# Performance work log

Measured on AMD Instinct MI355X. Metric: run time of the kernel, lower is better.

Reference implementation:

```python
import jax, jax.numpy as jnp
import numpy as np
from jax import lax

T, B, H, Q = 4096, 64, 128, 1024
K = 31                 # convolution_filter_size
PAD = (K - 1) // 2     # alignment_conv_padding = 15
WL = 128               # window_length


def setup_inputs() -> dict:
    key = jax.random.key(0)
    ks = jax.random.split(key, 8)
    return {
        "encoded_tokens": jax.random.normal(ks[0], (T, B, H), jnp.float32),
        "tokens_mask": jnp.ones((B, T), dtype=bool),
        "num_tokens": jnp.full((B,), T, dtype=jnp.int32),
        "query": jax.random.normal(ks[1], (1, B, Q), jnp.float32),
        "cumulative_alignment": jax.random.uniform(ks[2], (B, T), jnp.float32),
        "initial_cumulative_alignment": jax.random.uniform(ks[3], (B, 1), jnp.float32),
        "window_start": jax.random.randint(ks[4], (B,), 0, T - WL, dtype=jnp.int32),
        "Wq": jax.random.normal(ks[5], (H, Q), jnp.float32) * 0.02,
        "bq": jnp.zeros((H,), jnp.float32),
        "conv_w": jax.random.normal(ks[6], (H, 1, K), jnp.float32) * 0.1,
        "conv_b": jnp.zeros((H,), jnp.float32),
        "v": jax.random.normal(ks[7], (H,), jnp.float32) * 0.1,
    }


def reference(encoded_tokens, tokens_mask, num_tokens, query,
              cumulative_alignment, initial_cumulative_alignment, window_start,
              Wq, bq, conv_w, conv_b, v):
    Tn, Bn, Hn = encoded_tokens.shape
    W = min(WL, Tn)

    # mask padded positions of cumulative alignment
    cum = jnp.where(tokens_mask, cumulative_alignment, 0.0)          # [B, T]

    # left-pad with initial_cumulative_alignment, right-pad with zeros
    left = jnp.broadcast_to(initial_cumulative_alignment[..., None], (Bn, 1, PAD))
    loc = jnp.concatenate([left, cum[:, None, :]], axis=-1)          # [B, 1, T+PAD]
    loc = jnp.pad(loc, ((0, 0), (0, 0), (0, PAD)))                   # [B, 1, T+2*PAD]

    # variable-offset windows (gather)
    win_idx = window_start[:, None] + jnp.arange(W)                  # [B, W]
    mask_w = jnp.take_along_axis(tokens_mask, win_idx, axis=1)       # [B, W]
    enc_w = jax.vmap(lambda e, s: lax.dynamic_slice_in_dim(e, s, W, axis=0),
                     in_axes=(1, 0), out_axes=1)(encoded_tokens, window_start)  # [W, B, H]
    loc_w = jax.vmap(lambda l, s: lax.dynamic_slice_in_dim(l, s, W + 2 * PAD, axis=0),
                     in_axes=(0, 0))(loc[:, 0, :], window_start)     # [B, W+2*PAD]

    # location conv (valid padding) -> [B, H, W]
    feats = lax.conv_general_dilated(loc_w[:, None, :], conv_w, (1,), 'VALID',
                                     dimension_numbers=('NCH', 'OIH', 'NCH'))
    feats = feats + conv_b[None, :, None]

    # query projection and additive scoring
    qp = query[0] @ Wq.T + bq                                        # [B, H]
    feats = jnp.tanh(feats + qp[:, :, None])                         # [B, H, W]
    score = jnp.einsum('bhw,h->bw', feats, v)                        # [B, W]
    score = jnp.where(mask_w, score, -jnp.inf)
    align_w = jax.nn.softmax(score, axis=1)                          # [B, W]

    # context over the window
    context = jnp.einsum('bw,wbh->bh', align_w, enc_w)               # [B, H]

    # scatter window alignment back to full length
    align_full = jnp.zeros((Bn, Tn), align_w.dtype).at[
        jnp.arange(Bn)[:, None], win_idx].set(align_w)               # [B, T]

    ws_new = jnp.argmax(align_full, axis=1).astype(num_tokens.dtype) - W // 2
    ws_new = jnp.maximum(jnp.minimum(ws_new, num_tokens - W), 0)

    cum_new = cum + align_full
    return context, cum_new, align_full, ws_new
```

## Files before the change

### kernel.cpp

```cpp
#include <hip/hip_runtime.h>

#define T_DIM 4096
#define B_DIM 64
#define H_DIM 128
#define Q_DIM 1024
#define K_DIM 31
#define PADC 15
#define WL 128
#define NT 512

__device__ __forceinline__ float fast_tanh(float x) {
    float xc = fminf(fmaxf(x, -15.f), 15.f);
    float e = __expf(2.f * xc);
    return (e - 1.f) * __builtin_amdgcn_rcpf(e + 1.f);
}

__global__ __launch_bounds__(NT) void lsa_kernel(
    const float* __restrict__ enc,
    const int*   __restrict__ num_tokens,
    const float* __restrict__ query,
    const float* __restrict__ cum,
    const float* __restrict__ init_cum,
    const int*   __restrict__ window_start,
    const float* __restrict__ Wq,
    const float* __restrict__ bq,
    const float* __restrict__ conv_w,
    const float* __restrict__ conv_b,
    const float* __restrict__ vvec,
    float* __restrict__ out)
{
    const int b   = blockIdx.x;
    const int tid = threadIdx.x;
    const int ws   = window_start[b];
    const int ntok = num_tokens[b];

    __shared__ float s_q[Q_DIM];
    __shared__ float s_enc[WL * H_DIM];
    __shared__ float s_loc[WL + 2 * PADC];
    __shared__ float s_convw[H_DIM * K_DIM];
    __shared__ float s_qpb[H_DIM];
    __shared__ float s_v[H_DIM];
    __shared__ float s_part[4 * WL];
    __shared__ float s_align[WL];

    const int p0 = tid * 8;
    const float4* cin = reinterpret_cast<const float4*>(cum + (size_t)b * T_DIM + p0);
    float4 c0 = cin[0], c1 = cin[1];

    #pragma unroll
    for (int i = 0; i < 8; ++i) {
        int idx = tid + i * NT;
        int w = idx >> 5, c = idx & 31;
        float4 v = *reinterpret_cast<const float4*>(
            enc + ((size_t)(ws + w) * B_DIM + b) * H_DIM + c * 4);
        *reinterpret_cast<float4*>(&s_enc[w * H_DIM + c * 4]) = v;
    }
    {
        const float2* q2 = reinterpret_cast<const float2*>(query + (size_t)b * Q_DIM);
        float2 v = q2[tid];
        s_q[2 * tid] = v.x; s_q[2 * tid + 1] = v.y;
    }
    for (int i = tid; i < H_DIM * K_DIM; i += NT) s_convw[i] = conv_w[i];
    if (tid < H_DIM) s_v[tid] = vvec[tid];
    if (tid < WL + 2 * PADC) {
        int p = ws + tid;
        float val;
        if (p < PADC) val = init_cum[b];
        else {
            int t = p - PADC;
            val = (t < T_DIM && t < ntok) ? cum[(size_t)b * T_DIM + t] : 0.f;
        }
        s_loc[tid] = val;
    }
    __syncthreads();

    {
        int h = tid >> 2, part = tid & 3;
        const float4* wrow = reinterpret_cast<const float4*>(Wq + (size_t)h * Q_DIM + part * 256);
        const float* qs = &s_q[part * 256];
        float acc = 0.f;
        #pragma unroll 8
        for (int i = 0; i < 64; ++i) {
            float4 w4 = wrow[i];
            acc += w4.x * qs[4 * i]     + w4.y * qs[4 * i + 1]
                 + w4.z * qs[4 * i + 2] + w4.w * qs[4 * i + 3];
        }
        acc += __shfl_xor(acc, 1);
        acc += __shfl_xor(acc, 2);
        if (part == 0) s_qpb[h] = acc + bq[h] + conv_b[h];
    }
    __syncthreads();

    {
        int w = tid & (WL - 1);
        int g = tid >> 7;
        float sc = 0.f;
        for (int hh = 0; hh < 32; ++hh) {
            int h = g * 32 + hh;
            float a = s_qpb[h];
            const float* cw = &s_convw[h * K_DIM];
            #pragma unroll
            for (int k = 0; k < K_DIM; ++k) a += s_loc[w + k] * cw[k];
            sc += s_v[h] * fast_tanh(a);
        }
        s_part[g * WL + w] = sc;
    }
    __syncthreads();

    if (tid < WL) {
        float sc = s_part[tid] + s_part[WL + tid] + s_part[2 * WL + tid] + s_part[3 * WL + tid];
        bool valid = (ws + tid) < ntok;
        s_align[tid] = valid ? sc : -__builtin_inff();
    }
    __syncthreads();

    if (tid < 64) {
        float a0 = s_align[tid], a1 = s_align[tid + 64];
        float m = fmaxf(a0, a1);
        for (int off = 32; off; off >>= 1) m = fmaxf(m, __shfl_xor(m, off));
        float e0 = __expf(a0 - m), e1 = __expf(a1 - m);
        float s = e0 + e1;
        for (int off = 32; off; off >>= 1) s += __shfl_xor(s, off);
        float inv = __builtin_amdgcn_rcpf(s);
        e0 *= inv; e1 *= inv;
        s_align[tid] = e0; s_align[tid + 64] = e1;
        float bv = e0; int bi = tid;
        if (e1 > bv) { bv = e1; bi = tid + 64; }
        for (int off = 32; off; off >>= 1) {
            float ov = __shfl_xor(bv, off);
            int   oi = __shfl_xor(bi, off);
            if (ov > bv || (ov == bv && oi < bi)) { bv = ov; bi = oi; }
        }
        if (tid == 0) {
            int wsn = ws + bi - WL / 2;
            int hi = ntok - WL;
            if (wsn > hi) wsn = hi;
            if (wsn < 0) wsn = 0;
            out[(size_t)B_DIM * H_DIM + 2 * (size_t)B_DIM * T_DIM + b] = (float)wsn;
        }
    }
    __syncthreads();

    {
        int h = tid & (H_DIM - 1);
        int g = tid >> 7;
        float acc = 0.f;
        #pragma unroll 8
        for (int wi = 0; wi < 32; ++wi) {
            int w = g * 32 + wi;
            acc += s_align[w] * s_enc[w * H_DIM + h];
        }
        s_part[g * H_DIM + h] = acc;
    }
    __syncthreads();
    if (tid < H_DIM) {
        float c = s_part[tid] + s_part[H_DIM + tid] + s_part[2 * H_DIM + tid] + s_part[3 * H_DIM + tid];
        out[(size_t)b * H_DIM + tid] = c;
    }

    {
        float* out_cum   = out + (size_t)B_DIM * H_DIM;
        float* out_align = out_cum + (size_t)B_DIM * T_DIM;
        float ci[8] = {c0.x, c0.y, c0.z, c0.w, c1.x, c1.y, c1.z, c1.w};
        float oc[8], oa[8];
        #pragma unroll
        for (int i = 0; i < 8; ++i) {
            int p = p0 + i;
            float c = (p < ntok) ? ci[i] : 0.f;
            float a = ((unsigned)(p - ws) < (unsigned)WL) ? s_align[p - ws] : 0.f;
            oc[i] = c + a;
            oa[i] = a;
        }
        float4* pc = reinterpret_cast<float4*>(out_cum   + (size_t)b * T_DIM + p0);
        float4* pa = reinterpret_cast<float4*>(out_align + (size_t)b * T_DIM + p0);
        pc[0] = make_float4(oc[0], oc[1], oc[2], oc[3]);
        pc[1] = make_float4(oc[4], oc[5], oc[6], oc[7]);
        pa[0] = make_float4(oa[0], oa[1], oa[2], oa[3]);
        pa[1] = make_float4(oa[4], oa[5], oa[6], oa[7]);
    }
}

extern "C" void kernel_launch(void* const* d_in, const int* in_sizes, int n_in,
                              void* d_out, int out_size, void* d_ws, size_t ws_size,
                              hipStream_t stream) {
    const float* enc  = (const float*)d_in[0];
    const int* ntok   = (const int*)d_in[2];
    const float* qry  = (const float*)d_in[3];
    const float* cum  = (const float*)d_in[4];
    const float* ic   = (const float*)d_in[5];
    const int* wstart = (const int*)d_in[6];
    const float* Wq   = (const float*)d_in[7];
    const float* bq   = (const float*)d_in[8];
    const float* cw   = (const float*)d_in[9];
    const float* cb   = (const float*)d_in[10];
    const float* vv   = (const float*)d_in[11];
    float* out        = (float*)d_out;

    lsa_kernel<<<B_DIM, NT, 0, stream>>>(enc, ntok, qry, cum, ic, wstart,
                                         Wq, bq, cw, cb, vv, out);
}
```

Before: 208.3 us.

## Async-load encoder window into LDS overlapping the score computation

Moves the encoder-window gather from the kernel prologue to after the query projection and issues it as direct global-to-LDS loads, so it can overlap with the convolution/tanh scoring phase. It also defers the cumulative-alignment register loads, vectorises the conv-weight staging to float4, and folds the score reduction into the softmax warp, removing one barrier. The risk is correctness of async LDS completion: the global_load_lds writes need a wait before s_enc is read, which here relies on later __syncthreads, and the LDS offset mapping per wave must match the row layout.

```diff
diff --git a/kernel.cpp b/kernel.cpp
--- a/kernel.cpp
+++ b/kernel.cpp
@@ -35,32 +35,24 @@
     const int ntok = num_tokens[b];
 
     __shared__ float s_q[Q_DIM];
-    __shared__ float s_enc[WL * H_DIM];
+    __shared__ __align__(16) float s_enc[WL * H_DIM];
     __shared__ float s_loc[WL + 2 * PADC];
-    __shared__ float s_convw[H_DIM * K_DIM];
+    __shared__ __align__(16) float s_convw[H_DIM * K_DIM];
     __shared__ float s_qpb[H_DIM];
     __shared__ float s_v[H_DIM];
     __shared__ float s_part[4 * WL];
     __shared__ float s_align[WL];
 
-    const int p0 = tid * 8;
-    const float4* cin = reinterpret_cast<const float4*>(cum + (size_t)b * T_DIM + p0);
-    float4 c0 = cin[0], c1 = cin[1];
-
-    #pragma unroll
-    for (int i = 0; i < 8; ++i) {
-        int idx = tid + i * NT;
-        int w = idx >> 5, c = idx & 31;
-        float4 v = *reinterpret_cast<const float4*>(
-            enc + ((size_t)(ws + w) * B_DIM + b) * H_DIM + c * 4);
-        *reinterpret_cast<float4*>(&s_enc[w * H_DIM + c * 4]) = v;
-    }
     {
         const float2* q2 = reinterpret_cast<const float2*>(query + (size_t)b * Q_DIM);
         float2 v = q2[tid];
         s_q[2 * tid] = v.x; s_q[2 * tid + 1] = v.y;
     }
-    for (int i = tid; i < H_DIM * K_DIM; i += NT) s_convw[i] = conv_w[i];
+    {
+        const float4* cw4 = reinterpret_cast<const float4*>(conv_w);
+        float4* sw4 = reinterpret_cast<float4*>(s_convw);
+        for (int i = tid; i < (H_DIM * K_DIM) / 4; i += NT) sw4[i] = cw4[i];
+    }
     if (tid < H_DIM) s_v[tid] = vvec[tid];
     if (tid < WL + 2 * PADC) {
         int p = ws + tid;
@@ -90,6 +82,24 @@
         if (part == 0) s_qpb[h] = acc + bq[h] + conv_b[h];
     }
     __syncthreads();
+
+    {
+        int wv = tid >> 6, lane = tid & 63;
+        #pragma unroll
+        for (int i = 0; i < 8; ++i) {
+            int ci = (wv << 9) + (i << 6) + lane;
+            int w = ci >> 5, c = ci & 31;
+            const float* src = enc + ((size_t)(ws + w) * B_DIM + b) * H_DIM + (c << 2);
+            __builtin_amdgcn_global_load_lds(
+                (const __attribute__((address_space(1))) uint32_t*)src,
+                (__attribute__((address_space(3))) uint32_t*)(
+                    reinterpret_cast<char*>(s_enc) + (wv << 13) + (i << 10)),
+                16, 0, 0);
+        }
+    }
+    const int p0 = tid * 8;
+    const float4* cin = reinterpret_cast<const float4*>(cum + (size_t)b * T_DIM + p0);
+    float4 c0 = cin[0], c1 = cin[1];
 
     {
         int w = tid & (WL - 1);
@@ -107,15 +117,13 @@
     }
     __syncthreads();
 
-    if (tid < WL) {
-        float sc = s_part[tid] + s_part[WL + tid] + s_part[2 * WL + tid] + s_part[3 * WL + tid];
-        bool valid = (ws + tid) < ntok;
-        s_align[tid] = valid ? sc : -__builtin_inff();
-    }
-    __syncthreads();
-
     if (tid < 64) {
-        float a0 = s_align[tid], a1 = s_align[tid + 64];
+        float a0 = s_part[tid]      + s_part[WL + tid]
+                 + s_part[2 * WL + tid]      + s_part[3 * WL + tid];
+        float a1 = s_part[tid + 64] + s_part[WL + tid + 64]
+                 + s_part[2 * WL + tid + 64] + s_part[3 * WL + tid + 64];
+        if ((ws + tid)      >= ntok) a0 = -__builtin_inff();
+        if ((ws + tid + 64) >= ntok) a1 = -__builtin_inff();
         float m = fmaxf(a0, a1);
         for (int off = 32; off; off >>= 1) m = fmaxf(m, __shfl_xor(m, off));
         float e0 = __expf(a0 - m), e1 = __expf(a1 - m);
```

Result: no change. 206.1 us (-1.0%).
